# Kernel tuning notes

Hardware: AMD Instinct MI355X
Metric: run time of the kernel (lower is better)

The kernel has to match this reference:

```python
import jax, jax.numpy as jnp
import numpy as np

EPS = 1e-6

def setup_inputs() -> dict:
    key = jax.random.key(0)
    k1, k2, k3 = jax.random.split(key, 3)
    B, N, D = 1, 2048, 1024
    x = jax.random.normal(k1, (B, N, D), dtype=jnp.float32)
    W_qvk = jax.random.normal(k2, (D, 3 * D), dtype=jnp.float32) * (D ** -0.5)
    b_qvk = jax.random.normal(k3, (3 * D,), dtype=jnp.float32) * 0.02
    return {"x": x, "W_qvk": W_qvk, "b_qvk": b_qvk, "head_num": 16}


def _forward(x, W_qvk, b_qvk, head_num):
    B, N, D = x.shape
    qvk = x @ W_qvk + b_qvk                       # (B, N, 3D)
    # torch.chunk order in source: q, v, k
    def to_heads(t):
        return t.reshape(B, N, head_num, D // head_num).transpose(0, 2, 1, 3)  # (B,h,N,e)
    q, v, k = (to_heads(t) for t in jnp.split(qvk, 3, axis=-1))
    e = q.shape[-1]
    # causal linear attention, bucket_size=1
    q = jax.nn.softmax(q, axis=-1) * (e ** -0.5)  # (B,h,N,e)
    k = jnp.exp(k)
    k_cumsum = jnp.cumsum(k, axis=2)              # (B,h,N,e)
    # per-position outer product k_i (x) v_i, then causal prefix-sum over N
    kv = jnp.einsum('bhnd,bhne->bhnde', k, v)     # (B,h,N,e,e)
    kv_cumsum = jnp.cumsum(kv, axis=2)            # (B,h,N,e,e)
    denom = jnp.einsum('bhnd,bhnd->bhn', q, k_cumsum + EPS)   # (B,h,N)
    out = jnp.einsum('bhnd,bhnde->bhne', q, kv_cumsum) / denom[..., None]
    # concat heads: (B,h,N,e) -> (B,N,D)
    return out.transpose(0, 2, 1, 3).reshape(B, N, D)


def reference(x, W_qvk, b_qvk, head_num):
    return _forward(x, W_qvk, b_qvk, head_num)
```

## Files before the change

### kernel.cpp

```cpp
#include <hip/hip_runtime.h>
#include <stdint.h>

#define NTOK 2048
#define NCH 32

typedef __attribute__((ext_vector_type(8))) short bf16x8;
typedef __attribute__((ext_vector_type(8))) unsigned short ushort8v;
typedef __attribute__((ext_vector_type(4))) float f32x4;

__device__ __forceinline__ unsigned short f2bf(float f) {
  unsigned u = __float_as_uint(f);
  u += 0x7fffu + ((u >> 16) & 1u);
  return (unsigned short)(u >> 16);
}
__device__ __forceinline__ float bf2f(unsigned short s) {
  return __uint_as_float(((unsigned)s) << 16);
}

__global__ __launch_bounds__(256) void k_prep_inputs(const float* __restrict__ x,
                                                     unsigned short* __restrict__ xb,
                                                     const float* __restrict__ W,
                                                     unsigned short* __restrict__ Wt) {
  int bid = blockIdx.x;
  if (bid < 2048) {
    int i = (bid * 256 + threadIdx.x) * 4;
    float4 v = *(const float4*)(x + i);
    ushort4 o = { f2bf(v.x), f2bf(v.y), f2bf(v.z), f2bf(v.w) };
    *(ushort4*)(xb + i) = o;
  } else {
    __shared__ float tile[32][33];
    int id = bid - 2048;
    int bx = id % 96, by = id / 96;
    int tx = threadIdx.x & 31, ty = threadIdx.x >> 5;
    int c0 = bx * 32;
    int r0 = by * 32;
#pragma unroll
    for (int j = 0; j < 32; j += 8)
      tile[ty + j][tx] = W[(size_t)(r0 + ty + j) * 3072 + c0 + tx];
    __syncthreads();
#pragma unroll
    for (int j = 0; j < 32; j += 8) {
      int oc = c0 + ty + j;
      int rowp = ((oc & 1023) >> 6) * 192 + (oc >> 10) * 64 + (oc & 63);
      Wt[(size_t)rowp * 1024 + r0 + tx] = f2bf(tile[tx][ty + j]);
    }
  }
}

__global__ __launch_bounds__(768, 1) void k_gemm_fused(const unsigned short* __restrict__ xb,
                                                       const unsigned short* __restrict__ wt,
                                                       const float* __restrict__ bias,
                                                       unsigned short* __restrict__ qh,
                                                       unsigned short* __restrict__ kh,
                                                       unsigned short* __restrict__ vt,
                                                       unsigned short* __restrict__ Sc,
                                                       float* __restrict__ zc) {
  __shared__ __align__(16) unsigned short As[3][128][64];
  __shared__ __align__(16) unsigned short Bs[3][192][64];
  const int t = threadIdx.x;
  const int lane = t & 63;
  const int wave = t >> 6;
  const int wr = wave / 3;
  const int wc = wave % 3;
  const int rowBase = blockIdx.y * 128;
  const int colBase = blockIdx.x * 192;
  const int fr = lane & 15;
  const int khalf = lane >> 4;

  const bool isA = t < 256;
  const int nL = isA ? 4 : 3;
  const int bstr = isA ? 16384 : 24576;
  const unsigned short* gsrc[4];
  char* ldst[4];
#pragma unroll
  for (int j = 0; j < 4; ++j) {
    int idx = isA ? (t + j * 256) : (t - 256 + j * 512);
    if (j >= nL) idx = 0;
    int row = idx >> 3;
    int ssl = (idx & 7) ^ (row & 7);
    gsrc[j] = (isA ? xb + (size_t)(rowBase + row) * 1024
                   : wt + (size_t)(colBase + row) * 1024) + ssl * 8;
    ldst[j] = (isA ? (char*)As : (char*)Bs) + idx * 16;
  }

#define STG(buf, kt0) do {                                                                \
    _Pragma("unroll")                                                                     \
    for (int j_ = 0; j_ < 4; ++j_)                                                        \
      if (j_ < nL)                                                                        \
        __builtin_amdgcn_global_load_lds(                                                 \
            (const __attribute__((address_space(1))) void*)(gsrc[j_] + (kt0) * 64),       \
            (__attribute__((address_space(3))) void*)(ldst[j_] + (buf) * bstr), 16, 0, 0);\
  } while (0)

#define VMW_STEADY() do {                                                                 \
    if (isA) asm volatile("s_waitcnt vmcnt(4)" ::: "memory");                             \
    else     asm volatile("s_waitcnt vmcnt(3)" ::: "memory");                             \
  } while (0)
#define VMCNT0() asm volatile("s_waitcnt vmcnt(0)" ::: "memory")
#define LGKM0()  asm volatile("s_waitcnt lgkmcnt(0)" ::: "memory")
#define BAR()    __builtin_amdgcn_s_barrier()

  f32x4 acc[2][4] = {};
  const int fs0 = khalf ^ (fr & 7);

#define LOAD_FRAGS(cur, af, bff) do {                                                     \
    _Pragma("unroll")                                                                     \
    for (int m = 0; m < 2; ++m) {                                                         \
      const unsigned short* r = &As[cur][wr * 32 + m * 16 + fr][0];                       \
      af[m][0] = *(const bf16x8*)(r + fs0 * 8);                                           \
      af[m][1] = *(const bf16x8*)(r + (fs0 ^ 4) * 8);                                     \
    }                                                                                     \
    _Pragma("unroll")                                                                     \
    for (int n = 0; n < 4; ++n) {                                                         \
      const unsigned short* r = &Bs[cur][wc * 64 + n * 16 + fr][0];                       \
      bff[n][0] = *(const bf16x8*)(r + fs0 * 8);                                          \
      bff[n][1] = *(const bf16x8*)(r + (fs0 ^ 4) * 8);                                    \
    }                                                                                     \
  } while (0)

#define DO_MFMA(af, bff) do {                                                             \
    _Pragma("unroll")                                                                     \
    for (int m = 0; m < 2; ++m)                                                           \
      _Pragma("unroll")                                                                   \
      for (int n = 0; n < 4; ++n) {                                                       \
        acc[m][n] = __builtin_amdgcn_mfma_f32_16x16x32_bf16(af[m][0], bff[n][0], acc[m][n], 0, 0, 0); \
        acc[m][n] = __builtin_amdgcn_mfma_f32_16x16x32_bf16(af[m][1], bff[n][1], acc[m][n], 0, 0, 0); \
      }                                                                                   \
  } while (0)

  STG(0, 0);
  STG(1, 1);
#pragma unroll 1
  for (int ktile = 0; ktile < 16; ++ktile) {
    const int cur = ktile % 3;
    if (ktile < 15) { VMW_STEADY(); }
    else            { VMCNT0(); }
    BAR();
    __builtin_amdgcn_sched_barrier(0);
    bf16x8 af[2][2], bff[4][2];
    LOAD_FRAGS(cur, af, bff);
    if (ktile < 14) STG((ktile + 2) % 3, ktile + 2);
    LGKM0();
    __builtin_amdgcn_sched_barrier(0);
    __builtin_amdgcn_s_setprio(1);
    DO_MFMA(af, bff);
    __builtin_amdgcn_s_setprio(0);
  }
#undef STG
#undef LOAD_FRAGS
#undef DO_MFMA

  BAR();
  unsigned short (*Lkv)[2][64][72] =
      reinterpret_cast<unsigned short (*)[2][64][72]>(&As[0][0][0]);

  const int g2 = khalf;
  const int ocol = lane & 15;
  const int region = wc;
  const int h = blockIdx.x;
  const int r0 = rowBase + wr * 32;
  const int cch = r0 >> 6;
  const int cq = wr >> 1;
  const int lbase = (wr & 1) * 32;
  float bv[4];
#pragma unroll
  for (int n = 0; n < 4; ++n) bv[n] = bias[region * 1024 + h * 64 + 16 * n + ocol];

  if (region == 0) {
#pragma unroll
    for (int m = 0; m < 2; ++m) {
#pragma unroll
      for (int i = 0; i < 4; ++i) {
        float v[4];
#pragma unroll
        for (int n = 0; n < 4; ++n) v[n] = acc[m][n][i] + bv[n];
        float mx = fmaxf(fmaxf(v[0], v[1]), fmaxf(v[2], v[3]));
#pragma unroll
        for (int off = 1; off <= 8; off <<= 1) mx = fmaxf(mx, __shfl_xor(mx, off));
        float s = 0.f;
#pragma unroll
        for (int n = 0; n < 4; ++n) { v[n] = __expf(v[n] - mx); s += v[n]; }
#pragma unroll
        for (int off = 1; off <= 8; off <<= 1) s += __shfl_xor(s, off);
        float inv = 0.125f / s;
        int tok = r0 + 16 * m + 4 * g2 + i;
        unsigned short* qrow = qh + ((size_t)h * NTOK + tok) * 64;
#pragma unroll
        for (int n = 0; n < 4; ++n) qrow[16 * n + ocol] = f2bf(v[n] * inv);
      }
    }
  } else if (region == 1) {
    unsigned short* vb = vt + (size_t)(h * NCH + cch) * 4096;
#pragma unroll
    for (int m = 0; m < 2; ++m) {
      int tl = lbase + 16 * m + 4 * g2;
#pragma unroll
      for (int n = 0; n < 4; ++n) {
        int e = 16 * n + ocol;
        ushort4 p = { f2bf(acc[m][n][0] + bv[n]), f2bf(acc[m][n][1] + bv[n]),
                      f2bf(acc[m][n][2] + bv[n]), f2bf(acc[m][n][3] + bv[n]) };
        *(ushort4*)&vb[(size_t)e * 64 + tl] = p;
        *(ushort4*)&Lkv[cq][1][e][tl] = p;
      }
    }
  } else {
#pragma unroll
    for (int m = 0; m < 2; ++m) {
      int tl = lbase + 16 * m + 4 * g2;
#pragma unroll
      for (int n = 0; n < 4; ++n) {
        int e = 16 * n + ocol;
        float kv[4];
#pragma unroll
        for (int i = 0; i < 4; ++i) kv[i] = __expf(acc[m][n][i] + bv[n]);
        ushort4 p = { f2bf(kv[0]), f2bf(kv[1]), f2bf(kv[2]), f2bf(kv[3]) };
        *(ushort4*)&Lkv[cq][0][e][tl] = p;
#pragma unroll
        for (int i = 0; i < 4; ++i)
          kh[((size_t)h * NTOK + r0 + 16 * m + 4 * g2 + i) * 64 + e] = p[i];
      }
    }
  }
  BAR();

  if (wave < 8) {
    const int q = wave >> 2;
    const int w4 = wave & 3;
    const int cchg = 2 * blockIdx.y + q;
    bf16x8 ka[2];
#pragma unroll
    for (int ks = 0; ks < 2; ++ks)
      ka[ks] = *(const bf16x8*)&Lkv[q][0][16 * w4 + fr][32 * ks + khalf * 8];
    f32x4 s4[4] = {};
#pragma unroll
    for (int nb = 0; nb < 4; ++nb)
#pragma unroll
      for (int ks = 0; ks < 2; ++ks) {
        bf16x8 vf = *(const bf16x8*)&Lkv[q][1][16 * nb + fr][32 * ks + khalf * 8];
        s4[nb] = __builtin_amdgcn_mfma_f32_16x16x32_bf16(ka[ks], vf, s4[nb], 0, 0, 0);
      }
    unsigned short* so = Sc + (size_t)(h * NCH + cchg) * 4096;
#pragma unroll
    for (int nb = 0; nb < 4; ++nb) {
      ushort4 o = { f2bf(s4[nb][0]), f2bf(s4[nb][1]), f2bf(s4[nb][2]), f2bf(s4[nb][3]) };
      *(ushort4*)&so[(size_t)(16 * nb + fr) * 64 + 16 * w4 + 4 * g2] = o;
    }
    if (w4 == 0) {
      float z = 0.f;
#pragma unroll
      for (int j = 0; j < 8; ++j) {
        bf16x8 kv = *(const bf16x8*)&Lkv[q][0][lane][j * 8];
#pragma unroll
        for (int e = 0; e < 8; ++e) z += bf2f((unsigned short)kv[e]);
      }
      zc[(size_t)(h * NCH + cchg) * 64 + lane] = z;
    }
  }
}

__global__ __launch_bounds__(256) void k_scan(const unsigned short* __restrict__ Sc,
                                              unsigned short* __restrict__ Sp,
                                              const float* __restrict__ zc,
                                              float* __restrict__ zp) {
  int b = blockIdx.x;
  if (b < 256) {
    int tg = b * 256 + threadIdx.x;
    int h = tg >> 12, e = tg & 4095;
    float run = 0.f;
    for (int c = 0; c < NCH; ++c) {
      size_t idx = (size_t)(h * NCH + c) * 4096 + e;
      float v = bf2f(Sc[idx]);
      Sp[idx] = f2bf(run);
      run += v;
    }
  } else {
#pragma unroll
    for (int j = 0; j < 4; ++j) {
      int s = threadIdx.x + j * 256;
      int h = s >> 6, d = s & 63;
      float run = 0.f;
      for (int c = 0; c < NCH; ++c) {
        size_t idx = (size_t)(h * NCH + c) * 64 + d;
        zp[idx] = run;
        run += zc[idx];
      }
    }
  }
}

__global__ __launch_bounds__(256) void k_attn(const unsigned short* __restrict__ qh,
                                              const unsigned short* __restrict__ kh,
                                              const unsigned short* __restrict__ vt,
                                              const unsigned short* __restrict__ Sp,
                                              const float* __restrict__ zp,
                                              float* __restrict__ out) {
  int h = blockIdx.x >> 5, c = blockIdx.x & 31;
  __shared__ __align__(16) unsigned short Qs[64][72], Ks[64][72], Vts[64][72], Sts[64][72], Ams[64][72];
  __shared__ __align__(16) float zs[64];
  __shared__ float denom[64];
  int t = threadIdx.x, lane = t & 63, w = t >> 6;
  int fr = lane & 15, g = lane >> 4, fko = g * 8;
  const unsigned short* qg = qh + ((size_t)h * NTOK + c * 64) * 64;
  const unsigned short* kg = kh + ((size_t)h * NTOK + c * 64) * 64;
  const unsigned short* vg = vt + (size_t)(h * NCH + c) * 4096;
  const unsigned short* sg = Sp + (size_t)(h * NCH + c) * 4096;
  for (int s = t; s < 512; s += 256) {
    int r = s >> 3, c8 = (s & 7) * 8;
    *(ushort8v*)&Qs[r][c8]  = *(const ushort8v*)&qg[r * 64 + c8];
    *(ushort8v*)&Ks[r][c8]  = *(const ushort8v*)&kg[r * 64 + c8];
    *(ushort8v*)&Vts[r][c8] = *(const ushort8v*)&vg[r * 64 + c8];
    *(ushort8v*)&Sts[r][c8] = *(const ushort8v*)&sg[r * 64 + c8];
  }
  if (t < 64) zs[t] = zp[(size_t)h * NCH * 64 + (size_t)c * 64 + t];
  __syncthreads();

  bf16x8 qa[2];
#pragma unroll
  for (int ks = 0; ks < 2; ++ks) qa[ks] = *(const bf16x8*)&Qs[16 * w + fr][32 * ks + fko];
  f32x4 a1[4] = {};
#pragma unroll
  for (int mb = 0; mb < 4; ++mb)
#pragma unroll
    for (int ks = 0; ks < 2; ++ks) {
      bf16x8 kf = *(const bf16x8*)&Ks[16 * mb + fr][32 * ks + fko];
      a1[mb] = __builtin_amdgcn_mfma_f32_16x16x32_bf16(qa[ks], kf, a1[mb], 0, 0, 0);
    }
#pragma unroll
  for (int i = 0; i < 4; ++i) {
    int n = 16 * w + 4 * g + i;
    ushort4 qv4 = *(const ushort4*)&Qs[n][fr * 4];
    float4  zv4 = *(const float4*)&zs[fr * 4];
    float rs = bf2f(qv4.x) * zv4.x + bf2f(qv4.y) * zv4.y +
               bf2f(qv4.z) * zv4.z + bf2f(qv4.w) * zv4.w;
#pragma unroll
    for (int mb = 0; mb < 4; ++mb) {
      int m = 16 * mb + fr;
      float v = (m <= n) ? a1[mb][i] : 0.f;
      a1[mb][i] = v;
      rs += v;
      Ams[n][16 * mb + fr] = f2bf(v);
    }
#pragma unroll
    for (int off = 1; off <= 8; off <<= 1) rs += __shfl_xor(rs, off);
    if (fr == 0) denom[n] = rs + 1.25e-7f;
  }
  __syncthreads();

  bf16x8 xa[4];
#pragma unroll
  for (int ks = 0; ks < 2; ++ks) {
    xa[ks]     = *(const bf16x8*)&Vts[16 * w + fr][32 * ks + fko];
    xa[2 + ks] = *(const bf16x8*)&Sts[16 * w + fr][32 * ks + fko];
  }
  f32x4 o4[4] = {};
#pragma unroll
  for (int nb = 0; nb < 4; ++nb)
#pragma unroll
    for (int ks = 0; ks < 2; ++ks) {
      bf16x8 afr = *(const bf16x8*)&Ams[16 * nb + fr][32 * ks + fko];
      o4[nb] = __builtin_amdgcn_mfma_f32_16x16x32_bf16(xa[ks], afr, o4[nb], 0, 0, 0);
      bf16x8 qfr = *(const bf16x8*)&Qs[16 * nb + fr][32 * ks + fko];
      o4[nb] = __builtin_amdgcn_mfma_f32_16x16x32_bf16(xa[2 + ks], qfr, o4[nb], 0, 0, 0);
    }
#pragma unroll
  for (int nb = 0; nb < 4; ++nb) {
    int n = 16 * nb + fr;
    float dv = denom[n];
    float4 res = { o4[nb][0] / dv, o4[nb][1] / dv, o4[nb][2] / dv, o4[nb][3] / dv };
    *(float4*)&out[(size_t)(c * 64 + n) * 1024 + h * 64 + 16 * w + 4 * g] = res;
  }
}

extern "C" void kernel_launch(void* const* d_in, const int* in_sizes, int n_in,
                              void* d_out, int out_size, void* d_ws, size_t ws_size,
                              hipStream_t stream) {
  (void)in_sizes; (void)n_in; (void)out_size; (void)ws_size;
  const float* x = (const float*)d_in[0];
  const float* W = (const float*)d_in[1];
  const float* b = (const float*)d_in[2];
  char* ws = (char*)d_ws;

  const size_t MB = 1024 * 1024;
  unsigned short* xb = (unsigned short*)(ws + 0);
  unsigned short* Wt = (unsigned short*)(ws + 4 * MB);
  unsigned short* qh = (unsigned short*)(ws + 10 * MB);
  unsigned short* kh = (unsigned short*)(ws + 14 * MB);
  unsigned short* vt = (unsigned short*)(ws + 18 * MB);
  unsigned short* Sc = (unsigned short*)(ws + 22 * MB);
  unsigned short* Sp = (unsigned short*)(ws + 26 * MB);
  float*          zc = (float*)(ws + 30 * MB);
  float*          zp = (float*)(ws + 30 * MB + 131072);

  k_prep_inputs<<<dim3(5120), dim3(256), 0, stream>>>(x, xb, W, Wt);
  k_gemm_fused<<<dim3(16, 16), dim3(768), 0, stream>>>(xb, Wt, b, qh, kh, vt, Sc, zc);
  k_scan<<<dim3(257), dim3(256), 0, stream>>>(Sc, Sp, zc, zp);
  k_attn<<<dim3(512), dim3(256), 0, stream>>>(qh, kh, vt, Sp, zp, (float*)d_out);
}
```

Measured before the change: 44.17 us.

## Process two chunks per attention block with register prefetch of second chunk

Each k_attn block now handles two consecutive 64-token chunks of a head instead of one, halving the grid to 256 blocks. The second chunk's Q, K, V^T, S tiles and z vector are loaded into registers at the start, overlapping that global-memory latency with the first chunk's compute, then written to shared memory after it finishes. This trades fewer blocks (256 on a GPU with many CUs, so lower parallelism) and higher register pressure for hidden load latency.

Result: no change. 45.04 us (+2.0%).

```diff
diff --git a/kernel.cpp b/kernel.cpp
--- a/kernel.cpp
+++ b/kernel.cpp
@@ -294,16 +294,19 @@
                                               const unsigned short* __restrict__ Sp,
                                               const float* __restrict__ zp,
                                               float* __restrict__ out) {
-  int h = blockIdx.x >> 5, c = blockIdx.x & 31;
+  int h = blockIdx.x >> 4, pr = blockIdx.x & 15;
+  int c0 = pr * 2;
   __shared__ __align__(16) unsigned short Qs[64][72], Ks[64][72], Vts[64][72], Sts[64][72], Ams[64][72];
   __shared__ __align__(16) float zs[64];
   __shared__ float denom[64];
   int t = threadIdx.x, lane = t & 63, w = t >> 6;
   int fr = lane & 15, g = lane >> 4, fko = g * 8;
-  const unsigned short* qg = qh + ((size_t)h * NTOK + c * 64) * 64;
-  const unsigned short* kg = kh + ((size_t)h * NTOK + c * 64) * 64;
-  const unsigned short* vg = vt + (size_t)(h * NCH + c) * 4096;
-  const unsigned short* sg = Sp + (size_t)(h * NCH + c) * 4096;
+  const unsigned short* qg = qh + ((size_t)h * NTOK + c0 * 64) * 64;
+  const unsigned short* kg = kh + ((size_t)h * NTOK + c0 * 64) * 64;
+  const unsigned short* vg = vt + (size_t)(h * NCH + c0) * 4096;
+  const unsigned short* sg = Sp + (size_t)(h * NCH + c0) * 4096;
+
+#pragma unroll
   for (int s = t; s < 512; s += 256) {
     int r = s >> 3, c8 = (s & 7) * 8;
     *(ushort8v*)&Qs[r][c8]  = *(const ushort8v*)&qg[r * 64 + c8];
@@ -311,63 +314,95 @@
     *(ushort8v*)&Vts[r][c8] = *(const ushort8v*)&vg[r * 64 + c8];
     *(ushort8v*)&Sts[r][c8] = *(const ushort8v*)&sg[r * 64 + c8];
   }
-  if (t < 64) zs[t] = zp[(size_t)h * NCH * 64 + (size_t)c * 64 + t];
+  if (t < 64) zs[t] = zp[(size_t)h * NCH * 64 + (size_t)c0 * 64 + t];
+
+  ushort8v pf[2][4];
+  float zf1 = 0.f;
+#pragma unroll
+  for (int ii = 0; ii < 2; ++ii) {
+    int s = t + ii * 256;
+    int r = s >> 3, c8 = (s & 7) * 8;
+    pf[ii][0] = *(const ushort8v*)&qg[4096 + r * 64 + c8];
+    pf[ii][1] = *(const ushort8v*)&kg[4096 + r * 64 + c8];
+    pf[ii][2] = *(const ushort8v*)&vg[4096 + r * 64 + c8];
+    pf[ii][3] = *(const ushort8v*)&sg[4096 + r * 64 + c8];
+  }
+  if (t < 64) zf1 = zp[(size_t)h * NCH * 64 + (size_t)(c0 + 1) * 64 + t];
   __syncthreads();
 
-  bf16x8 qa[2];
-#pragma unroll
-  for (int ks = 0; ks < 2; ++ks) qa[ks] = *(const bf16x8*)&Qs[16 * w + fr][32 * ks + fko];
-  f32x4 a1[4] = {};
-#pragma unroll
-  for (int mb = 0; mb < 4; ++mb)
+#pragma unroll 1
+  for (int half = 0; half < 2; ++half) {
+    const int c = c0 + half;
+    bf16x8 qa[2];
+#pragma unroll
+    for (int ks = 0; ks < 2; ++ks) qa[ks] = *(const bf16x8*)&Qs[16 * w + fr][32 * ks + fko];
+    f32x4 a1[4] = {};
+#pragma unroll
+    for (int mb = 0; mb < 4; ++mb)
+#pragma unroll
+      for (int ks = 0; ks < 2; ++ks) {
+        bf16x8 kf = *(const bf16x8*)&Ks[16 * mb + fr][32 * ks + fko];
+        a1[mb] = __builtin_amdgcn_mfma_f32_16x16x32_bf16(qa[ks], kf, a1[mb], 0, 0, 0);
+      }
+#pragma unroll
+    for (int i = 0; i < 4; ++i) {
+      int n = 16 * w + 4 * g + i;
+      ushort4 qv4 = *(const ushort4*)&Qs[n][fr * 4];
+      float4  zv4 = *(const float4*)&zs[fr * 4];
+      float rs = bf2f(qv4.x) * zv4.x + bf2f(qv4.y) * zv4.y +
+                 bf2f(qv4.z) * zv4.z + bf2f(qv4.w) * zv4.w;
+#pragma unroll
+      for (int mb = 0; mb < 4; ++mb) {
+        int m = 16 * mb + fr;
+        float v = (m <= n) ? a1[mb][i] : 0.f;
+        a1[mb][i] = v;
+        rs += v;
+        Ams[n][16 * mb + fr] = f2bf(v);
+      }
+#pragma unroll
+      for (int off = 1; off <= 8; off <<= 1) rs += __shfl_xor(rs, off);
+      if (fr == 0) denom[n] = rs + 1.25e-7f;
+    }
+    __syncthreads();
+
+    bf16x8 xa[4];
 #pragma unroll
     for (int ks = 0; ks < 2; ++ks) {
-      bf16x8 kf = *(const bf16x8*)&Ks[16 * mb + fr][32 * ks + fko];
-      a1[mb] = __builtin_amdgcn_mfma_f32_16x16x32_bf16(qa[ks], kf, a1[mb], 0, 0, 0);
-    }
-#pragma unroll
-  for (int i = 0; i < 4; ++i) {
-    int n = 16 * w + 4 * g + i;
-    ushort4 qv4 = *(const ushort4*)&Qs[n][fr * 4];
-    float4  zv4 = *(const float4*)&zs[fr * 4];
-    float rs = bf2f(qv4.x) * zv4.x + bf2f(qv4.y) * zv4.y +
-               bf2f(qv4.z) * zv4.z + bf2f(qv4.w) * zv4.w;
-#pragma unroll
-    for (int mb = 0; mb < 4; ++mb) {
-      int m = 16 * mb + fr;
-      float v = (m <= n) ? a1[mb][i] : 0.f;
-      a1[mb][i] = v;
-      rs += v;
-      Ams[n][16 * mb + fr] = f2bf(v);
-    }
-#pragma unroll
-    for (int off = 1; off <= 8; off <<= 1) rs += __shfl_xor(rs, off);
-    if (fr == 0) denom[n] = rs + 1.25e-7f;
-  }
-  __syncthreads();
-
-  bf16x8 xa[4];
-#pragma unroll
-  for (int ks = 0; ks < 2; ++ks) {
-    xa[ks]     = *(const bf16x8*)&Vts[16 * w + fr][32 * ks + fko];
-    xa[2 + ks] = *(const bf16x8*)&Sts[16 * w + fr][32 * ks + fko];
-  }
-  f32x4 o4[4] = {};
-#pragma unroll
-  for (int nb = 0; nb < 4; ++nb)
-#pragma unroll
-    for (int ks = 0; ks < 2; ++ks) {
-      bf16x8 afr = *(const bf16x8*)&Ams[16 * nb + fr][32 * ks + fko];
-      o4[nb] = __builtin_amdgcn_mfma_f32_16x16x32_bf16(xa[ks], afr, o4[nb], 0, 0, 0);
-      bf16x8 qfr = *(const bf16x8*)&Qs[16 * nb + fr][32 * ks + fko];
-      o4[nb] = __builtin_amdgcn_mfma_f32_16x16x32_bf16(xa[2 + ks], qfr, o4[nb], 0, 0, 0);
-    }
-#pragma unroll
-  for (int nb = 0; nb < 4; ++nb) {
-    int n = 16 * nb + fr;
-    float dv = denom[n];
-    float4 res = { o4[nb][0] / dv, o4[nb][1] / dv, o4[nb][2] / dv, o4[nb][3] / dv };
-    *(float4*)&out[(size_t)(c * 64 + n) * 1024 + h * 64 + 16 * w + 4 * g] = res;
+      xa[ks]     = *(const bf16x8*)&Vts[16 * w + fr][32 * ks + fko];
+      xa[2 + ks] = *(const bf16x8*)&Sts[16 * w + fr][32 * ks + fko];
+    }
+    f32x4 o4[4] = {};
+#pragma unroll
+    for (int nb = 0; nb < 4; ++nb)
+#pragma unroll
+      for (int ks = 0; ks < 2; ++ks) {
+        bf16x8 afr = *(const bf16x8*)&Ams[16 * nb + fr][32 * ks + fko];
+        o4[nb] = __builtin_amdgcn_mfma_f32_16x16x32_bf16(xa[ks], afr, o4[nb], 0, 0, 0);
+        bf16x8 qfr = *(const bf16x8*)&Qs[16 * nb + fr][32 * ks + fko];
+        o4[nb] = __builtin_amdgcn_mfma_f32_16x16x32_bf16(xa[2 + ks], qfr, o4[nb], 0, 0, 0);
+      }
+#pragma unroll
+    for (int nb = 0; nb < 4; ++nb) {
+      int n = 16 * nb + fr;
+      float dv = denom[n];
+      float4 res = { o4[nb][0] / dv, o4[nb][1] / dv, o4[nb][2] / dv, o4[nb][3] / dv };
+      *(float4*)&out[(size_t)(c * 64 + n) * 1024 + h * 64 + 16 * w + 4 * g] = res;
+    }
+
+    if (half == 0) {
+      __syncthreads();
+#pragma unroll
+      for (int ii = 0; ii < 2; ++ii) {
+        int s = t + ii * 256;
+        int r = s >> 3, c8 = (s & 7) * 8;
+        *(ushort8v*)&Qs[r][c8]  = pf[ii][0];
+        *(ushort8v*)&Ks[r][c8]  = pf[ii][1];
+        *(ushort8v*)&Vts[r][c8] = pf[ii][2];
+        *(ushort8v*)&Sts[r][c8] = pf[ii][3];
+      }
+      if (t < 64) zs[t] = zf1;
+      __syncthreads();
+    }
   }
 }
 
@@ -394,5 +429,5 @@
   k_prep_inputs<<<dim3(5120), dim3(256), 0, stream>>>(x, xb, W, Wt);
   k_gemm_fused<<<dim3(16, 16), dim3(768), 0, stream>>>(xb, Wt, b, qh, kh, vt, Sc, zc);
   k_scan<<<dim3(257), dim3(256), 0, stream>>>(Sc, Sp, zc, zp);
-  k_attn<<<dim3(512), dim3(256), 0, stream>>>(qh, kh, vt, Sp, zp, (float*)d_out);
-}
+  k_attn<<<dim3(256), dim3(256), 0, stream>>>(qh, kh, vt, Sp, zp, (float*)d_out);
+}
```

## Load GEMM A fragments directly from global into registers, stage only B in LDS

Applied to the files above, without the earlier changes.

The fused QKV GEMM no longer stages the x tile through shared memory. Each wave loads its A fragments straight from global memory into registers, double-buffered across k-tiles, while all 768 threads share the B (weight) LDS staging. This cuts LDS footprint and LDS traffic and spreads the B loads over more threads. In exchange, A rows are re-read from global/L2 by the three waves sharing each row, and register pressure rises. The epilogue scratch now aliases Bs instead of the removed As.

New measurement: 60.67 us. 1.37x slower.

```diff
diff --git a/kernel.cpp b/kernel.cpp
--- a/kernel.cpp
+++ b/kernel.cpp
@@ -55,7 +55,6 @@
                                                        unsigned short* __restrict__ vt,
                                                        unsigned short* __restrict__ Sc,
                                                        float* __restrict__ zc) {
-  __shared__ __align__(16) unsigned short As[3][128][64];
   __shared__ __align__(16) unsigned short Bs[3][192][64];
   const int t = threadIdx.x;
   const int lane = t & 63;
@@ -67,49 +66,46 @@
   const int fr = lane & 15;
   const int khalf = lane >> 4;
 
-  const bool isA = t < 256;
-  const int nL = isA ? 4 : 3;
-  const int bstr = isA ? 16384 : 24576;
-  const unsigned short* gsrc[4];
-  char* ldst[4];
-#pragma unroll
-  for (int j = 0; j < 4; ++j) {
-    int idx = isA ? (t + j * 256) : (t - 256 + j * 512);
-    if (j >= nL) idx = 0;
+  const unsigned short* gB[2];
+  char* lB[2];
+#pragma unroll
+  for (int j = 0; j < 2; ++j) {
+    int idx = t + j * 768;
     int row = idx >> 3;
-    int ssl = (idx & 7) ^ (row & 7);
-    gsrc[j] = (isA ? xb + (size_t)(rowBase + row) * 1024
-                   : wt + (size_t)(colBase + row) * 1024) + ssl * 8;
-    ldst[j] = (isA ? (char*)As : (char*)Bs) + idx * 16;
-  }
-
-#define STG(buf, kt0) do {                                                                \
+    int slot = (idx & 7) ^ (row & 7);
+    gB[j] = wt + (size_t)(colBase + row) * 1024 + slot * 8;
+    lB[j] = (char*)Bs + idx * 16;
+  }
+  const unsigned short* aptr[2];
+#pragma unroll
+  for (int m = 0; m < 2; ++m)
+    aptr[m] = xb + (size_t)(rowBase + wr * 32 + m * 16 + fr) * 1024 + khalf * 8;
+
+#define STGB(buf, kt0) do {                                                               \
     _Pragma("unroll")                                                                     \
-    for (int j_ = 0; j_ < 4; ++j_)                                                        \
-      if (j_ < nL)                                                                        \
-        __builtin_amdgcn_global_load_lds(                                                 \
-            (const __attribute__((address_space(1))) void*)(gsrc[j_] + (kt0) * 64),       \
-            (__attribute__((address_space(3))) void*)(ldst[j_] + (buf) * bstr), 16, 0, 0);\
+    for (int j_ = 0; j_ < 2; ++j_)                                                        \
+      __builtin_amdgcn_global_load_lds(                                                   \
+          (const __attribute__((address_space(1))) void*)(gB[j_] + (kt0) * 64),           \
+          (__attribute__((address_space(3))) void*)(lB[j_] + (buf) * 24576), 16, 0, 0);   \
   } while (0)
 
-#define VMW_STEADY() do {                                                                 \
-    if (isA) asm volatile("s_waitcnt vmcnt(4)" ::: "memory");                             \
-    else     asm volatile("s_waitcnt vmcnt(3)" ::: "memory");                             \
+#define LOADA(dst, kt0) do {                                                              \
+    _Pragma("unroll")                                                                     \
+    for (int m_ = 0; m_ < 2; ++m_) {                                                      \
+      dst[m_][0] = *(const bf16x8*)(aptr[m_] + (kt0) * 64);                               \
+      dst[m_][1] = *(const bf16x8*)(aptr[m_] + (kt0) * 64 + 32);                          \
+    }                                                                                     \
   } while (0)
-#define VMCNT0() asm volatile("s_waitcnt vmcnt(0)" ::: "memory")
-#define LGKM0()  asm volatile("s_waitcnt lgkmcnt(0)" ::: "memory")
-#define BAR()    __builtin_amdgcn_s_barrier()
+
+#define VM2()   asm volatile("s_waitcnt vmcnt(2)" ::: "memory")
+#define VM0()   asm volatile("s_waitcnt vmcnt(0)" ::: "memory")
+#define LGKM0() asm volatile("s_waitcnt lgkmcnt(0)" ::: "memory")
+#define BAR()   __builtin_amdgcn_s_barrier()
 
   f32x4 acc[2][4] = {};
   const int fs0 = khalf ^ (fr & 7);
 
-#define LOAD_FRAGS(cur, af, bff) do {                                                     \
-    _Pragma("unroll")                                                                     \
-    for (int m = 0; m < 2; ++m) {                                                         \
-      const unsigned short* r = &As[cur][wr * 32 + m * 16 + fr][0];                       \
-      af[m][0] = *(const bf16x8*)(r + fs0 * 8);                                           \
-      af[m][1] = *(const bf16x8*)(r + (fs0 ^ 4) * 8);                                     \
-    }                                                                                     \
+#define LOADB(cur, bff) do {                                                              \
     _Pragma("unroll")                                                                     \
     for (int n = 0; n < 4; ++n) {                                                         \
       const unsigned short* r = &Bs[cur][wc * 64 + n * 16 + fr][0];                       \
@@ -128,31 +124,56 @@
       }                                                                                   \
   } while (0)
 
-  STG(0, 0);
-  STG(1, 1);
+  bf16x8 aA[2][2], aB[2][2];
+  LOADA(aA, 0);
+  STGB(0, 0);
+  STGB(1, 1);
 #pragma unroll 1
-  for (int ktile = 0; ktile < 16; ++ktile) {
-    const int cur = ktile % 3;
-    if (ktile < 15) { VMW_STEADY(); }
-    else            { VMCNT0(); }
-    BAR();
-    __builtin_amdgcn_sched_barrier(0);
-    bf16x8 af[2][2], bff[4][2];
-    LOAD_FRAGS(cur, af, bff);
-    if (ktile < 14) STG((ktile + 2) % 3, ktile + 2);
-    LGKM0();
-    __builtin_amdgcn_sched_barrier(0);
-    __builtin_amdgcn_s_setprio(1);
-    DO_MFMA(af, bff);
-    __builtin_amdgcn_s_setprio(0);
-  }
-#undef STG
-#undef LOAD_FRAGS
+  for (int kp = 0; kp < 8; ++kp) {
+    {
+      const int ktile = 2 * kp;
+      const int cur = ktile % 3;
+      VM2();
+      BAR();
+      __builtin_amdgcn_sched_barrier(0);
+      LOADA(aB, ktile + 1);
+      __builtin_amdgcn_sched_barrier(0);
+      if (ktile < 14) STGB((ktile + 2) % 3, ktile + 2);
+      bf16x8 bff[4][2];
+      LOADB(cur, bff);
+      LGKM0();
+      __builtin_amdgcn_sched_barrier(0);
+      __builtin_amdgcn_s_setprio(1);
+      DO_MFMA(aA, bff);
+      __builtin_amdgcn_s_setprio(0);
+    }
+    {
+      const int ktile = 2 * kp + 1;
+      const int cur = ktile % 3;
+      if (ktile < 15) { VM2(); }
+      else            { VM0(); }
+      BAR();
+      __builtin_amdgcn_sched_barrier(0);
+      if (ktile < 15) LOADA(aA, ktile + 1);
+      __builtin_amdgcn_sched_barrier(0);
+      if (ktile < 14) STGB((ktile + 2) % 3, ktile + 2);
+      bf16x8 bff[4][2];
+      LOADB(cur, bff);
+      LGKM0();
+      __builtin_amdgcn_sched_barrier(0);
+      __builtin_amdgcn_s_setprio(1);
+      DO_MFMA(aB, bff);
+      __builtin_amdgcn_s_setprio(0);
+    }
+  }
+#undef STGB
+#undef LOADA
+#undef LOADB
 #undef DO_MFMA
 
   BAR();
   unsigned short (*Lkv)[2][64][72] =
-      reinterpret_cast<unsigned short (*)[2][64][72]>(&As[0][0][0]);
+      reinterpret_cast<unsigned short (*)[2][64][72]>(&Bs[0][0][0]);
 
   const int g2 = khalf;
   const int ocol = lane & 15;
```
